# Kernel tuning notes

Hardware: AMD Instinct MI355X
Metric: run time of the kernel (lower is better)

## Reference

```python
import jax, jax.numpy as jnp
import numpy as np

N = 100000      # nodes
E = 640000      # directed edges (before self-loops)
F_IN = 128      # num_features
C1 = 64         # latent_size (conv1 out, heads=1)
C2 = 16         # num_classes (conv2 out, heads=1)
NEG_SLOPE = 0.2


def setup_inputs() -> dict:
    key = jax.random.key(0)
    ks = jax.random.split(key, 10)
    s = 0.1
    return {
        "x": jax.random.normal(ks[0], (N, F_IN), jnp.float32),
        "edge_index": jax.random.randint(ks[1], (2, E), 0, N, dtype=jnp.int32),
        "W1": jax.random.normal(ks[2], (F_IN, C1), jnp.float32) * s,
        "att_src1": jax.random.normal(ks[3], (C1,), jnp.float32) * s,
        "att_dst1": jax.random.normal(ks[4], (C1,), jnp.float32) * s,
        "b1": jax.random.normal(ks[5], (C1,), jnp.float32) * s,
        "W2": jax.random.normal(ks[6], (C1, C2), jnp.float32) * s,
        "att_src2": jax.random.normal(ks[7], (C2,), jnp.float32) * s,
        "att_dst2": jax.random.normal(ks[8], (C2,), jnp.float32) * s,
        "b2": jax.random.normal(ks[9], (C2,), jnp.float32) * s,
    }


def gat_layer(x, src, dst, W, a_src, a_dst, b, n_nodes):
    # x: [N, F] -> h: [N, C] (heads=1)
    h = x @ W
    # per-edge attention logits: alpha_j + alpha_i, then leaky_relu
    alpha = jax.nn.leaky_relu((h @ a_src)[src] + (h @ a_dst)[dst], NEG_SLOPE)
    # scatter-softmax over destination-node groups (numerically stable)
    amax = jax.ops.segment_max(alpha, dst, num_segments=n_nodes)
    e = jnp.exp(alpha - amax[dst])
    denom = jax.ops.segment_sum(e, dst, num_segments=n_nodes)
    w = e / (denom[dst] + 1e-16)
    # gather src features, weight, scatter-add to dst
    out = jax.ops.segment_sum(h[src] * w[:, None], dst, num_segments=n_nodes)
    return out + b


def kl_to_std_normal(out):
    # GIB reparameterize: mean = out[:, :ceil(C/2)], std = softplus(out[:, -ceil(C/2):])
    size = (out.shape[-1] + 1) // 2
    mean = out[:, :size]
    std = jax.nn.softplus(out[:, -size:]) + 1e-10
    kl = -jnp.log(std) + 0.5 * (std * std + mean * mean - 1.0)
    return kl.reshape(out.shape[0], -1, 1)  # [N, size, heads=1]


def reference(x, edge_index, W1, att_src1, att_dst1, b1, W2, att_src2, att_dst2, b2):
    n = x.shape[0]
    loop = jnp.arange(n, dtype=edge_index.dtype)  # PyG GATConv add_self_loops=True
    src = jnp.concatenate([edge_index[0], loop])
    dst = jnp.concatenate([edge_index[1], loop])

    out1 = gat_layer(x, src, dst, W1, att_src1, att_dst1, b1, n)
    ixz1 = kl_to_std_normal(out1)

    h = jax.nn.elu(out1)  # dropout is a no-op in eval mode
    out2 = gat_layer(h, src, dst, W2, att_src2, att_dst2, b2, n)
    ixz2 = kl_to_std_normal(out2)

    return (out2, ixz1, ixz2)
```

## Files before the change

kernel.cpp:

```cpp
#include <hip/hip_runtime.h>
#include <math.h>

#define NN 100000
#define NE 640000
#define ET (NE + NN)
#define FIN 128
#define C1 64
#define C2 16
#define NEG_SLOPE 0.2f
#define SLOTS 32
#define G1_BLOCKS ((NN + 127) / 128)
#define SCAT_BLOCKS ((ET + 255) / 256)

typedef unsigned int uint32;
typedef __attribute__((ext_vector_type(8))) short bf16x8;
typedef __attribute__((ext_vector_type(4))) float f32x4;

static __device__ __forceinline__ float lrelu(float x) { return x > 0.f ? x : NEG_SLOPE * x; }
static __device__ __forceinline__ float softplusf(float x) {
    return fmaxf(x, 0.f) + log1pf(expf(-fabsf(x)));
}
static __device__ __forceinline__ unsigned short f2bf(float f) {
    uint32 u = __float_as_uint(f);
    u += 0x7fffu + ((u >> 16) & 1u);
    return (unsigned short)(u >> 16);
}
static __device__ __forceinline__ float bf2f_lo(uint32 p) { return __uint_as_float(p << 16); }
static __device__ __forceinline__ float bf2f_hi(uint32 p) { return __uint_as_float(p & 0xffff0000u); }

#define G1T 2
__global__ __launch_bounds__(256, 3) void k_g1hist(
        const float* __restrict__ x, const float* __restrict__ W1,
        const float* __restrict__ attS, const float* __restrict__ attD,
        unsigned short* __restrict__ h1b, float* __restrict__ as1, float* __restrict__ ad1,
        const int* __restrict__ ei, int* __restrict__ cnt, int* __restrict__ csr32) {
    __shared__ uint32 ts[4][16][36];
    if (blockIdx.x >= G1_BLOCKS) {
        int i = (int)(blockIdx.x - G1_BLOCKS) * 256 + threadIdx.x;
        if (i < ET) {
            int src, dst;
            if (i < NE) { src = ei[i]; dst = ei[NE + i]; }
            else        { src = i - NE; dst = src; }
            int pos = atomicAdd(&cnt[dst], 1);
            if (pos < SLOTS) csr32[dst * SLOTS + pos] = src;
        }
        return;
    }
    int lane = threadIdx.x & 63;
    int wv = threadIdx.x >> 6;
    int col = lane & 15;
    int g = lane >> 4;
    int wbase = (blockIdx.x * 4 + wv) * (G1T * 16);
    if (wbase >= NN) return;

    bf16x8 bfr[4][4];
#pragma unroll
    for (int t = 0; t < 4; t++)
#pragma unroll
        for (int j = 0; j < 4; j++) {
            int c = col + j * 16;
#pragma unroll
            for (int i = 0; i < 8; i++)
                bfr[t][j][i] = (short)f2bf(W1[(t * 32 + g * 8 + i) * C1 + c]);
        }
    float ats[4], atd[4];
#pragma unroll
    for (int j = 0; j < 4; j++) { ats[j] = attS[col + j * 16]; atd[j] = attD[col + j * 16]; }

    for (int tl = 0; tl < G1T; tl++) {
        int tbase = wbase + tl * 16;
        int arow = tbase + col; if (arow > NN - 1) arow = NN - 1;
        const float* xr = &x[(size_t)arow * FIN];
        float4 f0[4], f1[4];
#pragma unroll
        for (int t = 0; t < 4; t++) {
            f0[t] = *reinterpret_cast<const float4*>(&xr[t * 32 + g * 8]);
            f1[t] = *reinterpret_cast<const float4*>(&xr[t * 32 + g * 8 + 4]);
        }
        bf16x8 a[4];
#pragma unroll
        for (int t = 0; t < 4; t++) {
            a[t][0] = (short)f2bf(f0[t].x); a[t][1] = (short)f2bf(f0[t].y);
            a[t][2] = (short)f2bf(f0[t].z); a[t][3] = (short)f2bf(f0[t].w);
            a[t][4] = (short)f2bf(f1[t].x); a[t][5] = (short)f2bf(f1[t].y);
            a[t][6] = (short)f2bf(f1[t].z); a[t][7] = (short)f2bf(f1[t].w);
        }
        f32x4 acc[4];
#pragma unroll
        for (int j = 0; j < 4; j++) acc[j] = (f32x4){0.f, 0.f, 0.f, 0.f};
#pragma unroll
        for (int t = 0; t < 4; t++)
#pragma unroll
            for (int j = 0; j < 4; j++)
                acc[j] = __builtin_amdgcn_mfma_f32_16x16x32_bf16(a[t], bfr[t][j], acc[j], 0, 0, 0);

        float sA[4] = {0.f, 0.f, 0.f, 0.f}, sD[4] = {0.f, 0.f, 0.f, 0.f};
        unsigned short* tsw = (unsigned short*)&ts[wv][0][0];
#pragma unroll
        for (int reg = 0; reg < 4; reg++) {
            int trow = g * 4 + reg;
#pragma unroll
            for (int j = 0; j < 4; j++) {
                float v = acc[j][reg];
                tsw[trow * 72 + col + j * 16] = f2bf(v);
                sA[reg] = fmaf(v, ats[j], sA[reg]);
                sD[reg] = fmaf(v, atd[j], sD[reg]);
            }
        }
        __builtin_amdgcn_wave_barrier();
        {
            int rrow = lane >> 2, rq = lane & 3;
            uint4 w0 = *reinterpret_cast<const uint4*>(&ts[wv][rrow][rq * 8]);
            uint4 w1 = *reinterpret_cast<const uint4*>(&ts[wv][rrow][rq * 8 + 4]);
            int orow = tbase + rrow;
            if (orow < NN) {
                unsigned short* op = &h1b[(size_t)orow * C1 + rq * 16];
                *reinterpret_cast<uint4*>(op) = w0;
                *reinterpret_cast<uint4*>(op + 8) = w1;
            }
        }
        __builtin_amdgcn_wave_barrier();
#pragma unroll
        for (int off = 8; off; off >>= 1)
#pragma unroll
            for (int reg = 0; reg < 4; reg++) {
                sA[reg] += __shfl_xor(sA[reg], off);
                sD[reg] += __shfl_xor(sD[reg], off);
            }
        if (col == 0) {
#pragma unroll
            for (int reg = 0; reg < 4; reg++) {
                int row = tbase + g * 4 + reg;
                if (row < NN) { as1[row] = sA[reg]; ad1[row] = sD[reg]; }
            }
        }
    }
}

__global__ __launch_bounds__(256, 4) void k_agg1(
        const int* __restrict__ cnt, const int* __restrict__ csr32,
        const float* __restrict__ as1, const float* __restrict__ ad1,
        const unsigned short* __restrict__ h1b, const float* __restrict__ b1,
        unsigned short* __restrict__ heb, float* __restrict__ ixz1) {
    int lane = threadIdx.x & 63;
    int wid = (blockIdx.x * blockDim.x + threadIdx.x) >> 6;
    int grp = lane >> 4, gl = lane & 15;
    int gbase = grp << 4;
    int node = wid * 4 + grp;
    if (node >= NN) return;
    int base = node * SLOTS;
    int deg = cnt[node];
    int s_l = csr32[base + gl];
    int4 S0 = *reinterpret_cast<const int4*>(&csr32[base]);
    int4 S1 = *reinterpret_cast<const int4*>(&csr32[base + 4]);
    int4 S2 = *reinterpret_cast<const int4*>(&csr32[base + 8]);
    int4 S3 = *reinterpret_cast<const int4*>(&csr32[base + 12]);
    float adn = ad1[node];
    float asv = as1[s_l];
    const unsigned short* hb = h1b + gl * 4;
    uint2 P0  = *reinterpret_cast<const uint2*>(&hb[(size_t)S0.x * C1]);
    uint2 P1  = *reinterpret_cast<const uint2*>(&hb[(size_t)S0.y * C1]);
    uint2 P2  = *reinterpret_cast<const uint2*>(&hb[(size_t)S0.z * C1]);
    uint2 P3  = *reinterpret_cast<const uint2*>(&hb[(size_t)S0.w * C1]);
    uint2 P4  = *reinterpret_cast<const uint2*>(&hb[(size_t)S1.x * C1]);
    uint2 P5  = *reinterpret_cast<const uint2*>(&hb[(size_t)S1.y * C1]);
    uint2 P6  = *reinterpret_cast<const uint2*>(&hb[(size_t)S1.z * C1]);
    uint2 P7  = *reinterpret_cast<const uint2*>(&hb[(size_t)S1.w * C1]);
    uint2 P8  = *reinterpret_cast<const uint2*>(&hb[(size_t)S2.x * C1]);
    uint2 P9  = *reinterpret_cast<const uint2*>(&hb[(size_t)S2.y * C1]);
    uint2 P10 = *reinterpret_cast<const uint2*>(&hb[(size_t)S2.z * C1]);
    uint2 P11 = *reinterpret_cast<const uint2*>(&hb[(size_t)S2.w * C1]);
    uint2 P12 = *reinterpret_cast<const uint2*>(&hb[(size_t)S3.x * C1]);
    uint2 P13 = *reinterpret_cast<const uint2*>(&hb[(size_t)S3.y * C1]);
    uint2 P14 = *reinterpret_cast<const uint2*>(&hb[(size_t)S3.z * C1]);
    uint2 P15 = *reinterpret_cast<const uint2*>(&hb[(size_t)S3.w * C1]);
    __builtin_amdgcn_sched_barrier(0);
    float4 o;

    if (deg <= 16) {
        float al = (gl < deg) ? lrelu(asv + adn) : -1e30f;
        float wl = expf(al);
        float den = wl;
#pragma unroll
        for (int off = 8; off; off >>= 1) den += __shfl_xor(den, off);
        wl *= 1.f / (den + 1e-16f);
        float4 acc = make_float4(0.f, 0.f, 0.f, 0.f);
#define ACC1(k, Pk) { float w = __shfl(wl, gbase | k); \
        acc.x = fmaf(w, bf2f_lo(Pk.x), acc.x); acc.y = fmaf(w, bf2f_hi(Pk.x), acc.y); \
        acc.z = fmaf(w, bf2f_lo(Pk.y), acc.z); acc.w = fmaf(w, bf2f_hi(Pk.y), acc.w); }
        ACC1(0, P0)  ACC1(1, P1)  ACC1(2, P2)  ACC1(3, P3)
        ACC1(4, P4)  ACC1(5, P5)  ACC1(6, P6)  ACC1(7, P7)
        ACC1(8, P8)  ACC1(9, P9)  ACC1(10, P10) ACC1(11, P11)
        ACC1(12, P12) ACC1(13, P13) ACC1(14, P14) ACC1(15, P15)
#undef ACC1
        o = acc;
    } else {
        int dcl = deg < SLOTS ? deg : SLOTS;
        float m = -1e30f;
        for (int e = gl; e < dcl; e += 16) m = fmaxf(m, lrelu(as1[csr32[base + e]] + adn));
#pragma unroll
        for (int off = 8; off; off >>= 1) m = fmaxf(m, __shfl_xor(m, off));
        float den = 0.f;
        for (int e = gl; e < dcl; e += 16) den += expf(lrelu(as1[csr32[base + e]] + adn) - m);
#pragma unroll
        for (int off = 8; off; off >>= 1) den += __shfl_xor(den, off);
        float inv = 1.f / (den + 1e-16f);
        float4 acc = make_float4(0.f, 0.f, 0.f, 0.f);
        for (int e = 0; e < dcl; e++) {
            int s = csr32[base + e];
            float wgt = expf(lrelu(as1[s] + adn) - m) * inv;
            uint2 p = *reinterpret_cast<const uint2*>(&h1b[(size_t)s * C1 + gl * 4]);
            acc.x = fmaf(wgt, bf2f_lo(p.x), acc.x);
            acc.y = fmaf(wgt, bf2f_hi(p.x), acc.y);
            acc.z = fmaf(wgt, bf2f_lo(p.y), acc.z);
            acc.w = fmaf(wgt, bf2f_hi(p.y), acc.w);
        }
        o = acc;
    }
    float4 bv = *reinterpret_cast<const float4*>(&b1[gl * 4]);
    o.x += bv.x; o.y += bv.y; o.z += bv.z; o.w += bv.w;
    float4 he;
    he.x = o.x > 0.f ? o.x : expm1f(o.x);
    he.y = o.y > 0.f ? o.y : expm1f(o.y);
    he.z = o.z > 0.f ? o.z : expm1f(o.z);
    he.w = o.w > 0.f ? o.w : expm1f(o.w);
    uint2 hw;
    hw.x = (uint32)f2bf(he.x) | ((uint32)f2bf(he.y) << 16);
    hw.y = (uint32)f2bf(he.z) | ((uint32)f2bf(he.w) << 16);
    *reinterpret_cast<uint2*>(&heb[(size_t)node * C1 + gl * 4]) = hw;
    float4 oth;
    oth.x = __shfl_down(o.x, 8);
    oth.y = __shfl_down(o.y, 8);
    oth.z = __shfl_down(o.z, 8);
    oth.w = __shfl_down(o.w, 8);
    if (gl < 8) {
        float4 kl; float sd;
        sd = softplusf(oth.x) + 1e-10f; kl.x = -logf(sd) + 0.5f * (sd * sd + o.x * o.x - 1.f);
        sd = softplusf(oth.y) + 1e-10f; kl.y = -logf(sd) + 0.5f * (sd * sd + o.y * o.y - 1.f);
        sd = softplusf(oth.z) + 1e-10f; kl.z = -logf(sd) + 0.5f * (sd * sd + o.z * o.z - 1.f);
        sd = softplusf(oth.w) + 1e-10f; kl.w = -logf(sd) + 0.5f * (sd * sd + o.w * o.w - 1.f);
        *reinterpret_cast<float4*>(&ixz1[(size_t)node * 32 + gl * 4]) = kl;
    }
}

#define G2T 4
__global__ __launch_bounds__(256, 4) void k_gemm2(
        const unsigned short* __restrict__ heb, const float* __restrict__ W2,
        const float* __restrict__ attS, const float* __restrict__ attD,
        unsigned short* __restrict__ h2b, float* __restrict__ as2, float* __restrict__ ad2) {
    int lane = threadIdx.x & 63;
    int wv = threadIdx.x >> 6;
    int col = lane & 15, g = lane >> 4;
    int wbase = (blockIdx.x * 4 + wv) * (G2T * 16);
    if (wbase >= NN) return;
    bf16x8 bfr[2];
#pragma unroll
    for (int t = 0; t < 2; t++)
#pragma unroll
        for (int i = 0; i < 8; i++)
            bfr[t][i] = (short)f2bf(W2[(t * 32 + g * 8 + i) * C2 + col]);
    float ats = attS[col], atd = attD[col];
#pragma unroll
    for (int tl = 0; tl < G2T; tl++) {
        int tbase = wbase + tl * 16;
        if (tbase >= NN) break;
        int arow = tbase + col; if (arow > NN - 1) arow = NN - 1;
        bf16x8 a0 = *reinterpret_cast<const bf16x8*>(&heb[(size_t)arow * C1 + g * 8]);
        bf16x8 a1 = *reinterpret_cast<const bf16x8*>(&heb[(size_t)arow * C1 + 32 + g * 8]);
        f32x4 acc = (f32x4){0.f, 0.f, 0.f, 0.f};
        acc = __builtin_amdgcn_mfma_f32_16x16x32_bf16(a0, bfr[0], acc, 0, 0, 0);
        acc = __builtin_amdgcn_mfma_f32_16x16x32_bf16(a1, bfr[1], acc, 0, 0, 0);
        float sA[4], sD[4];
#pragma unroll
        for (int reg = 0; reg < 4; reg++) {
            int row = tbase + g * 4 + reg;
            if (row < NN) h2b[(size_t)row * C2 + col] = f2bf(acc[reg]);
            sA[reg] = acc[reg] * ats;
            sD[reg] = acc[reg] * atd;
        }
#pragma unroll
        for (int off = 8; off; off >>= 1)
#pragma unroll
            for (int reg = 0; reg < 4; reg++) {
                sA[reg] += __shfl_xor(sA[reg], off);
                sD[reg] += __shfl_xor(sD[reg], off);
            }
        if (col == 0) {
#pragma unroll
            for (int reg = 0; reg < 4; reg++) {
                int row = tbase + g * 4 + reg;
                if (row < NN) { as2[row] = sA[reg]; ad2[row] = sD[reg]; }
            }
        }
    }
}

__global__ __launch_bounds__(256, 8) void k_agg2(
        const int* __restrict__ cnt, const int* __restrict__ csr32,
        const float* __restrict__ as2, const float* __restrict__ ad2,
        const unsigned short* __restrict__ h2b, const float* __restrict__ b2,
        float* __restrict__ out2, float* __restrict__ ixz2) {
    int lane = threadIdx.x & 63;
    int wid = (blockIdx.x * blockDim.x + threadIdx.x) >> 6;
    int grp = lane >> 4, gl = lane & 15;
    int gbase = grp << 4;
    int node = wid * 4 + grp;
    if (node >= NN) return;
    int base = node * SLOTS;
    int f4 = gl & 3, eg = gl >> 2;
    int deg = cnt[node];
    int s_l = csr32[base + gl];
    int sk0 = csr32[base + eg];
    int sk1 = csr32[base + 4 + eg];
    int sk2 = csr32[base + 8 + eg];
    int sk3 = csr32[base + 12 + eg];
    float adn = ad2[node];
    float asv = as2[s_l];
    uint2 P0 = *reinterpret_cast<const uint2*>(&h2b[(size_t)sk0 * C2 + f4 * 4]);
    uint2 P1 = *reinterpret_cast<const uint2*>(&h2b[(size_t)sk1 * C2 + f4 * 4]);
    uint2 P2 = *reinterpret_cast<const uint2*>(&h2b[(size_t)sk2 * C2 + f4 * 4]);
    uint2 P3 = *reinterpret_cast<const uint2*>(&h2b[(size_t)sk3 * C2 + f4 * 4]);
    __builtin_amdgcn_sched_barrier(0);
    float out;

    if (deg <= 16) {
        float al = (gl < deg) ? lrelu(asv + adn) : -1e30f;
        float wl = expf(al);
        float den = wl;
#pragma unroll
        for (int off = 8; off; off >>= 1) den += __shfl_xor(den, off);
        wl *= 1.f / (den + 1e-16f);
        float4 acc = make_float4(0.f, 0.f, 0.f, 0.f);
        float w0 = __shfl(wl, gbase | eg);
        float w1 = __shfl(wl, gbase | (4 + eg));
        float w2 = __shfl(wl, gbase | (8 + eg));
        float w3 = __shfl(wl, gbase | (12 + eg));
        acc.x = fmaf(w0, bf2f_lo(P0.x), acc.x);
        acc.y = fmaf(w0, bf2f_hi(P0.x), acc.y);
        acc.z = fmaf(w0, bf2f_lo(P0.y), acc.z);
        acc.w = fmaf(w0, bf2f_hi(P0.y), acc.w);
        acc.x = fmaf(w1, bf2f_lo(P1.x), acc.x);
        acc.y = fmaf(w1, bf2f_hi(P1.x), acc.y);
        acc.z = fmaf(w1, bf2f_lo(P1.y), acc.z);
        acc.w = fmaf(w1, bf2f_hi(P1.y), acc.w);
        acc.x = fmaf(w2, bf2f_lo(P2.x), acc.x);
        acc.y = fmaf(w2, bf2f_hi(P2.x), acc.y);
        acc.z = fmaf(w2, bf2f_lo(P2.y), acc.z);
        acc.w = fmaf(w2, bf2f_hi(P2.y), acc.w);
        acc.x = fmaf(w3, bf2f_lo(P3.x), acc.x);
        acc.y = fmaf(w3, bf2f_hi(P3.x), acc.y);
        acc.z = fmaf(w3, bf2f_lo(P3.y), acc.z);
        acc.w = fmaf(w3, bf2f_hi(P3.y), acc.w);
#pragma unroll
        for (int off = 4; off <= 8; off <<= 1) {
            acc.x += __shfl_xor(acc.x, off);
            acc.y += __shfl_xor(acc.y, off);
            acc.z += __shfl_xor(acc.z, off);
            acc.w += __shfl_xor(acc.w, off);
        }
        int srcl = gbase | (gl >> 2);
        float t0 = __shfl(acc.x, srcl);
        float t1 = __shfl(acc.y, srcl);
        float t2 = __shfl(acc.z, srcl);
        float t3 = __shfl(acc.w, srcl);
        float t01 = (gl & 1) ? t1 : t0;
        float t23 = (gl & 1) ? t3 : t2;
        out = (gl & 2) ? t23 : t01;
    } else {
        int dcl = deg < SLOTS ? deg : SLOTS;
        float m = -1e30f;
        for (int e = gl; e < dcl; e += 16) m = fmaxf(m, lrelu(as2[csr32[base + e]] + adn));
#pragma unroll
        for (int off = 8; off; off >>= 1) m = fmaxf(m, __shfl_xor(m, off));
        float den = 0.f;
        for (int e = gl; e < dcl; e += 16) den += expf(lrelu(as2[csr32[base + e]] + adn) - m);
#pragma unroll
        for (int off = 8; off; off >>= 1) den += __shfl_xor(den, off);
        float inv = 1.f / (den + 1e-16f);
        float acc = 0.f;
        for (int e = 0; e < dcl; e++) {
            int s = csr32[base + e];
            float wgt = expf(lrelu(as2[s] + adn) - m) * inv;
            acc = fmaf(wgt, __uint_as_float(((uint32)h2b[(size_t)s * C2 + gl]) << 16), acc);
        }
        out = acc;
    }
    out += b2[gl];
    out2[(size_t)node * C2 + gl] = out;
    float other = __shfl_down(out, 8);
    if (gl < 8) {
        float sd = softplusf(other) + 1e-10f;
        float kl = -logf(sd) + 0.5f * (sd * sd + out * out - 1.f);
        ixz2[(size_t)node * 8 + gl] = kl;
    }
}

extern "C" void kernel_launch(void* const* d_in, const int* in_sizes, int n_in,
                              void* d_out, int out_size, void* d_ws, size_t ws_size,
                              hipStream_t stream) {
    const float* x     = (const float*)d_in[0];
    const int*   ei    = (const int*)d_in[1];
    const float* W1    = (const float*)d_in[2];
    const float* aS1   = (const float*)d_in[3];
    const float* aD1   = (const float*)d_in[4];
    const float* b1    = (const float*)d_in[5];
    const float* W2    = (const float*)d_in[6];
    const float* aS2   = (const float*)d_in[7];
    const float* aD2   = (const float*)d_in[8];
    const float* b2    = (const float*)d_in[9];

    float* out = (float*)d_out;
    float* out2 = out;
    float* ixz1 = out + (size_t)NN * C2;
    float* ixz2 = ixz1 + (size_t)NN * 32;

    char* p = (char*)d_ws;
    auto alloc = [&](size_t bytes) -> void* {
        void* r = (void*)p;
        p += (bytes + 255) & ~(size_t)255;
        return r;
    };
    int* cnt     = (int*)alloc((size_t)NN * 4);
    int* csr32   = (int*)alloc((size_t)NN * SLOTS * 4);
    unsigned short* h1b = (unsigned short*)alloc((size_t)NN * C1 * 2);
    float* as1   = (float*)alloc((size_t)NN * 4);
    float* ad1   = (float*)alloc((size_t)NN * 4);
    unsigned short* heb = (unsigned short*)alloc((size_t)NN * C1 * 2);
    unsigned short* h2b = (unsigned short*)alloc((size_t)NN * C2 * 2);
    float* as2   = (float*)alloc((size_t)NN * 4);
    float* ad2   = (float*)alloc((size_t)NN * 4);
    (void)ws_size; (void)in_sizes; (void)n_in; (void)out_size;

    hipMemsetAsync(cnt, 0, (size_t)((char*)h1b - (char*)cnt), stream);

    k_g1hist<<<G1_BLOCKS + SCAT_BLOCKS, 256, 0, stream>>>(x, W1, aS1, aD1, h1b, as1, ad1, ei, cnt, csr32);

    k_agg1<<<(NN + 15) / 16, 256, 0, stream>>>(cnt, csr32, as1, ad1, h1b, b1, heb, ixz1);

    k_gemm2<<<(NN + 4 * G2T * 16 - 1) / (4 * G2T * 16), 256, 0, stream>>>(heb, W2, aS2, aD2, h2b, as2, ad2);
    k_agg2<<<(NN + 15) / 16, 256, 0, stream>>>(cnt, csr32, as2, ad2, h2b, b2, out2, ixz2);
}
```

Measured before the change: 123.6 us.

## Handle self-loops implicitly and use fast intrinsic exp/log/rcp

Self-loop edges are no longer inserted into the per-destination slot lists by the histogram pass. Each aggregation instead loads the node's own feature row and adds its attention weight directly. This removes 100k atomic inserts, frees one slot per node, and puts more nodes on the fast degree-16 path. Precise expf, logf, expm1f, log1pf and division are replaced with __expf, __logf and rcp intrinsics, which lowers math cost at some loss of accuracy. The early gather loads now sit inside the branch instead of before a sched_barrier, which may reduce how much load latency is overlapped.

New measurement: 115.7 us. -6.4%, faster.

```diff
diff --git a/kernel.cpp b/kernel.cpp
--- a/kernel.cpp
+++ b/kernel.cpp
@@ -3,22 +3,21 @@
 
 #define NN 100000
 #define NE 640000
-#define ET (NE + NN)
 #define FIN 128
 #define C1 64
 #define C2 16
 #define NEG_SLOPE 0.2f
 #define SLOTS 32
 #define G1_BLOCKS ((NN + 127) / 128)
-#define SCAT_BLOCKS ((ET + 255) / 256)
+#define SCAT_BLOCKS ((NE + 255) / 256)
 
 typedef unsigned int uint32;
 typedef __attribute__((ext_vector_type(8))) short bf16x8;
 typedef __attribute__((ext_vector_type(4))) float f32x4;
 
 static __device__ __forceinline__ float lrelu(float x) { return x > 0.f ? x : NEG_SLOPE * x; }
-static __device__ __forceinline__ float softplusf(float x) {
-    return fmaxf(x, 0.f) + log1pf(expf(-fabsf(x)));
+static __device__ __forceinline__ float softplusn(float x) {
+    return fmaxf(x, 0.f) + __logf(1.f + __expf(-fabsf(x)));
 }
 static __device__ __forceinline__ unsigned short f2bf(float f) {
     uint32 u = __float_as_uint(f);
@@ -37,10 +36,8 @@
     __shared__ uint32 ts[4][16][36];
     if (blockIdx.x >= G1_BLOCKS) {
         int i = (int)(blockIdx.x - G1_BLOCKS) * 256 + threadIdx.x;
-        if (i < ET) {
-            int src, dst;
-            if (i < NE) { src = ei[i]; dst = ei[NE + i]; }
-            else        { src = i - NE; dst = src; }
+        if (i < NE) {
+            int src = ei[i], dst = ei[NE + i];
             int pos = atomicAdd(&cnt[dst], 1);
             if (pos < SLOTS) csr32[dst * SLOTS + pos] = src;
         }
@@ -149,42 +146,50 @@
     int node = wid * 4 + grp;
     if (node >= NN) return;
     int base = node * SLOTS;
-    int deg = cnt[node];
+    int dcnt = cnt[node];
     int s_l = csr32[base + gl];
     int4 S0 = *reinterpret_cast<const int4*>(&csr32[base]);
     int4 S1 = *reinterpret_cast<const int4*>(&csr32[base + 4]);
     int4 S2 = *reinterpret_cast<const int4*>(&csr32[base + 8]);
     int4 S3 = *reinterpret_cast<const int4*>(&csr32[base + 12]);
     float adn = ad1[node];
+    float asn = as1[node];
     float asv = as1[s_l];
-    const unsigned short* hb = h1b + gl * 4;
-    uint2 P0  = *reinterpret_cast<const uint2*>(&hb[(size_t)S0.x * C1]);
-    uint2 P1  = *reinterpret_cast<const uint2*>(&hb[(size_t)S0.y * C1]);
-    uint2 P2  = *reinterpret_cast<const uint2*>(&hb[(size_t)S0.z * C1]);
-    uint2 P3  = *reinterpret_cast<const uint2*>(&hb[(size_t)S0.w * C1]);
-    uint2 P4  = *reinterpret_cast<const uint2*>(&hb[(size_t)S1.x * C1]);
-    uint2 P5  = *reinterpret_cast<const uint2*>(&hb[(size_t)S1.y * C1]);
-    uint2 P6  = *reinterpret_cast<const uint2*>(&hb[(size_t)S1.z * C1]);
-    uint2 P7  = *reinterpret_cast<const uint2*>(&hb[(size_t)S1.w * C1]);
-    uint2 P8  = *reinterpret_cast<const uint2*>(&hb[(size_t)S2.x * C1]);
-    uint2 P9  = *reinterpret_cast<const uint2*>(&hb[(size_t)S2.y * C1]);
-    uint2 P10 = *reinterpret_cast<const uint2*>(&hb[(size_t)S2.z * C1]);
-    uint2 P11 = *reinterpret_cast<const uint2*>(&hb[(size_t)S2.w * C1]);
-    uint2 P12 = *reinterpret_cast<const uint2*>(&hb[(size_t)S3.x * C1]);
-    uint2 P13 = *reinterpret_cast<const uint2*>(&hb[(size_t)S3.y * C1]);
-    uint2 P14 = *reinterpret_cast<const uint2*>(&hb[(size_t)S3.z * C1]);
-    uint2 P15 = *reinterpret_cast<const uint2*>(&hb[(size_t)S3.w * C1]);
-    __builtin_amdgcn_sched_barrier(0);
     float4 o;
 
-    if (deg <= 16) {
-        float al = (gl < deg) ? lrelu(asv + adn) : -1e30f;
-        float wl = expf(al);
+    if (dcnt <= 16) {
+        float al = (gl < dcnt) ? lrelu(asv + adn) : -1e30f;
+        float wl = __expf(al);
         float den = wl;
 #pragma unroll
         for (int off = 8; off; off >>= 1) den += __shfl_xor(den, off);
-        wl *= 1.f / (den + 1e-16f);
-        float4 acc = make_float4(0.f, 0.f, 0.f, 0.f);
+        float wself = __expf(lrelu(asn + adn));
+        den += wself;
+        float inv = __builtin_amdgcn_rcpf(den + 1e-16f);
+        wl *= inv; wself *= inv;
+        const unsigned short* hb = h1b + gl * 4;
+        uint2 PS  = *reinterpret_cast<const uint2*>(&hb[(size_t)node * C1]);
+        uint2 P0  = *reinterpret_cast<const uint2*>(&hb[(size_t)S0.x * C1]);
+        uint2 P1  = *reinterpret_cast<const uint2*>(&hb[(size_t)S0.y * C1]);
+        uint2 P2  = *reinterpret_cast<const uint2*>(&hb[(size_t)S0.z * C1]);
+        uint2 P3  = *reinterpret_cast<const uint2*>(&hb[(size_t)S0.w * C1]);
+        uint2 P4  = *reinterpret_cast<const uint2*>(&hb[(size_t)S1.x * C1]);
+        uint2 P5  = *reinterpret_cast<const uint2*>(&hb[(size_t)S1.y * C1]);
+        uint2 P6  = *reinterpret_cast<const uint2*>(&hb[(size_t)S1.z * C1]);
+        uint2 P7  = *reinterpret_cast<const uint2*>(&hb[(size_t)S1.w * C1]);
+        uint2 P8  = *reinterpret_cast<const uint2*>(&hb[(size_t)S2.x * C1]);
+        uint2 P9  = *reinterpret_cast<const uint2*>(&hb[(size_t)S2.y * C1]);
+        uint2 P10 = *reinterpret_cast<const uint2*>(&hb[(size_t)S2.z * C1]);
+        uint2 P11 = *reinterpret_cast<const uint2*>(&hb[(size_t)S2.w * C1]);
+        uint2 P12 = *reinterpret_cast<const uint2*>(&hb[(size_t)S3.x * C1]);
+        uint2 P13 = *reinterpret_cast<const uint2*>(&hb[(size_t)S3.y * C1]);
+        uint2 P14 = *reinterpret_cast<const uint2*>(&hb[(size_t)S3.z * C1]);
+        uint2 P15 = *reinterpret_cast<const uint2*>(&hb[(size_t)S3.w * C1]);
+        float4 acc;
+        acc.x = wself * bf2f_lo(PS.x);
+        acc.y = wself * bf2f_hi(PS.x);
+        acc.z = wself * bf2f_lo(PS.y);
+        acc.w = wself * bf2f_hi(PS.y);
 #define ACC1(k, Pk) { float w = __shfl(wl, gbase | k); \
         acc.x = fmaf(w, bf2f_lo(Pk.x), acc.x); acc.y = fmaf(w, bf2f_hi(Pk.x), acc.y); \
         acc.z = fmaf(w, bf2f_lo(Pk.y), acc.z); acc.w = fmaf(w, bf2f_hi(Pk.y), acc.w); }
@@ -195,20 +200,28 @@
 #undef ACC1
         o = acc;
     } else {
-        int dcl = deg < SLOTS ? deg : SLOTS;
-        float m = -1e30f;
+        int dcl = dcnt < SLOTS ? dcnt : SLOTS;
+        float aself = lrelu(asn + adn);
+        float m = aself;
         for (int e = gl; e < dcl; e += 16) m = fmaxf(m, lrelu(as1[csr32[base + e]] + adn));
 #pragma unroll
         for (int off = 8; off; off >>= 1) m = fmaxf(m, __shfl_xor(m, off));
         float den = 0.f;
-        for (int e = gl; e < dcl; e += 16) den += expf(lrelu(as1[csr32[base + e]] + adn) - m);
+        for (int e = gl; e < dcl; e += 16) den += __expf(lrelu(as1[csr32[base + e]] + adn) - m);
 #pragma unroll
         for (int off = 8; off; off >>= 1) den += __shfl_xor(den, off);
-        float inv = 1.f / (den + 1e-16f);
-        float4 acc = make_float4(0.f, 0.f, 0.f, 0.f);
+        den += __expf(aself - m);
+        float inv = __builtin_amdgcn_rcpf(den + 1e-16f);
+        float wsf = __expf(aself - m) * inv;
+        uint2 ps = *reinterpret_cast<const uint2*>(&h1b[(size_t)node * C1 + gl * 4]);
+        float4 acc;
+        acc.x = wsf * bf2f_lo(ps.x);
+        acc.y = wsf * bf2f_hi(ps.x);
+        acc.z = wsf * bf2f_lo(ps.y);
+        acc.w = wsf * bf2f_hi(ps.y);
         for (int e = 0; e < dcl; e++) {
             int s = csr32[base + e];
-            float wgt = expf(lrelu(as1[s] + adn) - m) * inv;
+            float wgt = __expf(lrelu(as1[s] + adn) - m) * inv;
             uint2 p = *reinterpret_cast<const uint2*>(&h1b[(size_t)s * C1 + gl * 4]);
             acc.x = fmaf(wgt, bf2f_lo(p.x), acc.x);
             acc.y = fmaf(wgt, bf2f_hi(p.x), acc.y);
@@ -220,10 +233,10 @@
     float4 bv = *reinterpret_cast<const float4*>(&b1[gl * 4]);
     o.x += bv.x; o.y += bv.y; o.z += bv.z; o.w += bv.w;
     float4 he;
-    he.x = o.x > 0.f ? o.x : expm1f(o.x);
-    he.y = o.y > 0.f ? o.y : expm1f(o.y);
-    he.z = o.z > 0.f ? o.z : expm1f(o.z);
-    he.w = o.w > 0.f ? o.w : expm1f(o.w);
+    he.x = o.x > 0.f ? o.x : __expf(o.x) - 1.f;
+    he.y = o.y > 0.f ? o.y : __expf(o.y) - 1.f;
+    he.z = o.z > 0.f ? o.z : __expf(o.z) - 1.f;
+    he.w = o.w > 0.f ? o.w : __expf(o.w) - 1.f;
     uint2 hw;
     hw.x = (uint32)f2bf(he.x) | ((uint32)f2bf(he.y) << 16);
     hw.y = (uint32)f2bf(he.z) | ((uint32)f2bf(he.w) << 16);
@@ -235,10 +248,10 @@
     oth.w = __shfl_down(o.w, 8);
     if (gl < 8) {
         float4 kl; float sd;
-        sd = softplusf(oth.x) + 1e-10f; kl.x = -logf(sd) + 0.5f * (sd * sd + o.x * o.x - 1.f);
-        sd = softplusf(oth.y) + 1e-10f; kl.y = -logf(sd) + 0.5f * (sd * sd + o.y * o.y - 1.f);
-        sd = softplusf(oth.z) + 1e-10f; kl.z = -logf(sd) + 0.5f * (sd * sd + o.z * o.z - 1.f);
-        sd = softplusf(oth.w) + 1e-10f; kl.w = -logf(sd) + 0.5f * (sd * sd + o.w * o.w - 1.f);
+        sd = softplusn(oth.x) + 1e-10f; kl.x = -__logf(sd) + 0.5f * (sd * sd + o.x * o.x - 1.f);
+        sd = softplusn(oth.y) + 1e-10f; kl.y = -__logf(sd) + 0.5f * (sd * sd + o.y * o.y - 1.f);
+        sd = softplusn(oth.z) + 1e-10f; kl.z = -__logf(sd) + 0.5f * (sd * sd + o.z * o.z - 1.f);
+        sd = softplusn(oth.w) + 1e-10f; kl.w = -__logf(sd) + 0.5f * (sd * sd + o.w * o.w - 1.f);
         *reinterpret_cast<float4*>(&ixz1[(size_t)node * 32 + gl * 4]) = kl;
     }
 }
@@ -308,29 +321,38 @@
     if (node >= NN) return;
     int base = node * SLOTS;
     int f4 = gl & 3, eg = gl >> 2;
-    int deg = cnt[node];
+    int dcnt = cnt[node];
     int s_l = csr32[base + gl];
     int sk0 = csr32[base + eg];
     int sk1 = csr32[base + 4 + eg];
     int sk2 = csr32[base + 8 + eg];
     int sk3 = csr32[base + 12 + eg];
     float adn = ad2[node];
+    float asn = as2[node];
     float asv = as2[s_l];
-    uint2 P0 = *reinterpret_cast<const uint2*>(&h2b[(size_t)sk0 * C2 + f4 * 4]);
-    uint2 P1 = *reinterpret_cast<const uint2*>(&h2b[(size_t)sk1 * C2 + f4 * 4]);
-    uint2 P2 = *reinterpret_cast<const uint2*>(&h2b[(size_t)sk2 * C2 + f4 * 4]);
-    uint2 P3 = *reinterpret_cast<const uint2*>(&h2b[(size_t)sk3 * C2 + f4 * 4]);
-    __builtin_amdgcn_sched_barrier(0);
     float out;
 
-    if (deg <= 16) {
-        float al = (gl < deg) ? lrelu(asv + adn) : -1e30f;
-        float wl = expf(al);
+    if (dcnt <= 16) {
+        float al = (gl < dcnt) ? lrelu(asv + adn) : -1e30f;
+        float wl = __expf(al);
         float den = wl;
 #pragma unroll
         for (int off = 8; off; off >>= 1) den += __shfl_xor(den, off);
-        wl *= 1.f / (den + 1e-16f);
-        float4 acc = make_float4(0.f, 0.f, 0.f, 0.f);
+        float wself = __expf(lrelu(asn + adn));
+        den += wself;
+        float inv = __builtin_amdgcn_rcpf(den + 1e-16f);
+        wl *= inv; wself *= inv;
+        uint2 PS = *reinterpret_cast<const uint2*>(&h2b[(size_t)node * C2 + f4 * 4]);
+        uint2 P0 = *reinterpret_cast<const uint2*>(&h2b[(size_t)sk0 * C2 + f4 * 4]);
+        uint2 P1 = *reinterpret_cast<const uint2*>(&h2b[(size_t)sk1 * C2 + f4 * 4]);
+        uint2 P2 = *reinterpret_cast<const uint2*>(&h2b[(size_t)sk2 * C2 + f4 * 4]);
+        uint2 P3 = *reinterpret_cast<const uint2*>(&h2b[(size_t)sk3 * C2 + f4 * 4]);
+        float ws = (eg == 0) ? wself : 0.f;
+        float4 acc;
+        acc.x = ws * bf2f_lo(PS.x);
+        acc.y = ws * bf2f_hi(PS.x);
+        acc.z = ws * bf2f_lo(PS.y);
+        acc.w = ws * bf2f_hi(PS.y);
         float w0 = __shfl(wl, gbase | eg);
         float w1 = __shfl(wl, gbase | (4 + eg));
         float w2 = __shfl(wl, gbase | (8 + eg));
@@ -367,20 +389,23 @@
         float t23 = (gl & 1) ? t3 : t2;
         out = (gl & 2) ? t23 : t01;
     } else {
-        int dcl = deg < SLOTS ? deg : SLOTS;
-        float m = -1e30f;
+        int dcl = dcnt < SLOTS ? dcnt : SLOTS;
+        float aself = lrelu(asn + adn);
+        float m = aself;
         for (int e = gl; e < dcl; e += 16) m = fmaxf(m, lrelu(as2[csr32[base + e]] + adn));
 #pragma unroll
         for (int off = 8; off; off >>= 1) m = fmaxf(m, __shfl_xor(m, off));
         float den = 0.f;
-        for (int e = gl; e < dcl; e += 16) den += expf(lrelu(as2[csr32[base + e]] + adn) - m);
+        for (int e = gl; e < dcl; e += 16) den += __expf(lrelu(as2[csr32[base + e]] + adn) - m);
 #pragma unroll
         for (int off = 8; off; off >>= 1) den += __shfl_xor(den, off);
-        float inv = 1.f / (den + 1e-16f);
-        float acc = 0.f;
+        den += __expf(aself - m);
+        float inv = __builtin_amdgcn_rcpf(den + 1e-16f);
+        float wsf = __expf(aself - m) * inv;
+        float acc = wsf * __uint_as_float(((uint32)h2b[(size_t)node * C2 + gl]) << 16);
         for (int e = 0; e < dcl; e++) {
             int s = csr32[base + e];
-            float wgt = expf(lrelu(as2[s] + adn) - m) * inv;
+            float wgt = __expf(lrelu(as2[s] + adn) - m) * inv;
             acc = fmaf(wgt, __uint_as_float(((uint32)h2b[(size_t)s * C2 + gl]) << 16), acc);
         }
         out = acc;
@@ -389,8 +414,8 @@
     out2[(size_t)node * C2 + gl] = out;
     float other = __shfl_down(out, 8);
     if (gl < 8) {
-        float sd = softplusf(other) + 1e-10f;
-        float kl = -logf(sd) + 0.5f * (sd * sd + out * out - 1.f);
+        float sd = softplusn(other) + 1e-10f;
+        float kl = -__logf(sd) + 0.5f * (sd * sd + out * out - 1.f);
         ixz2[(size_t)node * 8 + gl] = kl;
     }
 }
```
